# Performance work log

Hardware: AMD Instinct MI355X
Metric: run time of the kernel (lower is better)

## Reference

```python
import jax, jax.numpy as jnp
import numpy as np

B, C, H, W = 16, 512, 32, 32
NUM_HEADS = 8
GROUPS = 32
EPS = 1e-5


def setup_inputs() -> dict:
    key = jax.random.key(0)
    ks = jax.random.split(key, 3)
    x = jax.random.normal(ks[0], (B, C, H, W), dtype=jnp.float32)
    # Conv2d 1x1 weights stored as (out, in); init ~ fan-in scaled normal
    qkv_w = jax.random.normal(ks[1], (3 * C, C), dtype=jnp.float32) * (C ** -0.5)
    proj_w = jax.random.normal(ks[2], (C, C), dtype=jnp.float32) * (C ** -0.5)
    return {
        "x": x,
        "norm_w": jnp.ones((C,), jnp.float32),
        "norm_b": jnp.zeros((C,), jnp.float32),
        "qkv_w": qkv_w,
        "qkv_b": jnp.zeros((3 * C,), jnp.float32),
        "proj_w": proj_w,
        "proj_b": jnp.zeros((C,), jnp.float32),
    }


def reference(x, norm_w, norm_b, qkv_w, qkv_b, proj_w, proj_b):
    b, c, hh, ww = x.shape
    nh = NUM_HEADS
    hd = c // nh
    n = hh * ww

    # GroupNorm(32, C)
    xg = x.reshape(b, GROUPS, c // GROUPS, hh, ww)
    mean = xg.mean(axis=(2, 3, 4), keepdims=True)
    var = ((xg - mean) ** 2).mean(axis=(2, 3, 4), keepdims=True)
    hn = ((xg - mean) * jax.lax.rsqrt(var + EPS)).reshape(b, c, hh, ww)
    hn = hn * norm_w[None, :, None, None] + norm_b[None, :, None, None]

    # 1x1 conv QKV projection
    qkv = jnp.einsum('bchw,oc->bohw', hn, qkv_w) + qkv_b[None, :, None, None]
    # (B,3C,H,W) -> (B,3,nh,hd,N) -> (3,B,nh,N,hd)
    qkv = qkv.reshape(b, 3, nh, hd, n).transpose(1, 0, 2, 4, 3)
    q, k, v = qkv[0], qkv[1], qkv[2]

    scale = hd ** -0.5
    attn = jax.nn.softmax(jnp.einsum('bhnd,bhmd->bhnm', q, k) * scale, axis=-1)
    o = jnp.einsum('bhnm,bhmd->bhnd', attn, v)  # (B,nh,N,hd)
    o = o.transpose(0, 1, 3, 2).reshape(b, c, hh, ww)

    out = jnp.einsum('bchw,oc->bohw', o, proj_w) + proj_b[None, :, None, None]
    return out + x
```

## Files before the change

kernel.cpp:

```cpp
#include <hip/hip_runtime.h>
#include <cstdint>
#include <math.h>


typedef __bf16 bf16;
typedef __attribute__((ext_vector_type(8))) __bf16 bf16x8;
typedef __attribute__((ext_vector_type(4))) float f32x4;
typedef __attribute__((ext_vector_type(4))) short s16x4;

union U8 { uint4 u4; bf16x8 v; bf16 h[8]; };
union U4 { ushort4 u; bf16 h[4]; };
union UB4 { ushort4 u; s16x4 s; bf16 h[4]; };
union F4 { float4 v; float f[4]; };

typedef __attribute__((address_space(1))) void* gp1;
typedef __attribute__((address_space(3))) void* lp3;

__device__ __forceinline__ void async16(const void* g, void* l) {
  __builtin_amdgcn_global_load_lds((gp1)g, (lp3)l, 16, 0, 0);
}

#define LOG2E 1.44269504f

__global__ __launch_bounds__(256) void cvt_w(const float* __restrict__ qw,
                                             const float* __restrict__ pw,
                                             bf16* __restrict__ qwb,
                                             bf16* __restrict__ pwb) {
  int i = blockIdx.x * 256 + threadIdx.x;
  F4 v; bf16* dst;
  if (i < 196608) { v.v = ((const float4*)qw)[i]; dst = qwb + (size_t)i * 4; }
  else { v.v = ((const float4*)pw)[i - 196608]; dst = pwb + (size_t)(i - 196608) * 4; }
  U4 o;
#pragma unroll
  for (int j = 0; j < 4; j++) o.h[j] = (bf16)v.f[j];
  *(ushort4*)dst = o.u;
}

__global__ __launch_bounds__(256) void gn_stats(const float* __restrict__ x,
                                                float2* __restrict__ stats) {
  int bg = blockIdx.x;
  const float* base = x + (size_t)bg * 16384;
  int t = threadIdx.x;
  float s = 0.f, ss = 0.f;
#pragma unroll
  for (int p = 0; p < 16; p++) {
    F4 u; u.v = *(const float4*)(base + (size_t)(p * 256 + t) * 4);
#pragma unroll
    for (int i = 0; i < 4; i++) { float v = u.f[i]; s += v; ss += v * v; }
  }
  for (int off = 1; off < 64; off <<= 1) { s += __shfl_xor(s, off); ss += __shfl_xor(ss, off); }
  __shared__ float red[8];
  int w = t >> 6;
  if ((t & 63) == 0) { red[w] = s; red[4 + w] = ss; }
  __syncthreads();
  if (t == 0) {
    float S = red[0] + red[1] + red[2] + red[3];
    float SS = red[4] + red[5] + red[6] + red[7];
    float mean = S * (1.f / 16384.f);
    float var = SS * (1.f / 16384.f) - mean * mean;
    stats[bg] = make_float2(mean, rsqrtf(var + 1e-5f));
  }
}

__global__ __launch_bounds__(256) void gn_apply(const float* __restrict__ x,
                                                const float* __restrict__ nwp,
                                                const float* __restrict__ nbp,
                                                const float2* __restrict__ stats,
                                                bf16* __restrict__ hnt) {
  int b = blockIdx.z, nt = blockIdx.y, ct = blockIdx.x;
  int t = threadIdx.x, w = t >> 6, l = t & 63;
  int wc = w & 1, wn = w >> 1;
  int cb = ct * 128 + wc * 64 + (l & 7) * 8;
  int n0 = nt * 64 + wn * 32 + (l >> 3) * 4;
  float2 ms = stats[b * 32 + (cb >> 4)];
  float wgt[8], bia[8];
#pragma unroll
  for (int i = 0; i < 8; i++) {
    float wi = nwp[cb + i] * ms.y;
    wgt[i] = wi;
    bia[i] = nbp[cb + i] - ms.x * wi;
  }
  F4 in[8];
  const float* xb = x + ((size_t)b * 512 + cb) * 1024 + n0;
#pragma unroll
  for (int i = 0; i < 8; i++) in[i].v = *(const float4*)(xb + (size_t)i * 1024);
  bf16* ob = hnt + ((size_t)b * 1024 + n0) * 512 + cb;
#pragma unroll
  for (int j = 0; j < 4; j++) {
    U8 o;
#pragma unroll
    for (int i = 0; i < 8; i++) o.h[i] = (bf16)(in[i].f[j] * wgt[i] + bia[i]);
    *(uint4*)(ob + (size_t)j * 512) = o.u4;
  }
}

__device__ __forceinline__ void gemm_bt_core(const bf16* ga0, const bf16* gb0,
                                             bf16* At, bf16* Bt,
                                             f32x4 (&acc)[4][4], int w, int l) {
  const bf16* ga = ga0 + (size_t)(w * 16 + (l >> 2)) * 512 + (l & 3) * 8;
  const bf16* gb = gb0 + (size_t)(w * 16 + (l >> 2)) * 512 + (l & 3) * 8;
  int wr = w >> 1, wc = w & 1;
  const bf16* Ab = At + (wr * 64 + (l & 15)) * 32 + (l >> 4) * 8;
  const bf16* Bb = Bt + (wc * 64 + (l & 15)) * 32 + (l >> 4) * 8;
  bf16* lA = At + w * 16 * 32;
  bf16* lB = Bt + w * 16 * 32;
  for (int k0 = 0; k0 < 512; k0 += 32) {
    async16(ga + k0, lA);
    async16(ga + 64 * 512 + k0, lA + 64 * 32);
    async16(gb + k0, lB);
    async16(gb + 64 * 512 + k0, lB + 64 * 32);
    __syncthreads();
    bf16x8 af[4], bfr[4];
#pragma unroll
    for (int i = 0; i < 4; i++) {
      af[i] = *(const bf16x8*)(Ab + i * 512);
      bfr[i] = *(const bf16x8*)(Bb + i * 512);
    }
#pragma unroll
    for (int i = 0; i < 4; i++)
#pragma unroll
      for (int j = 0; j < 4; j++)
        acc[i][j] = __builtin_amdgcn_mfma_f32_16x16x32_bf16(af[i], bfr[j], acc[i][j], 0, 0, 0);
    __syncthreads();
  }
}

__global__ __launch_bounds__(256, 2) void qkv_gemm(const bf16* __restrict__ hnt,
                                                   const bf16* __restrict__ qwb,
                                                   const float* __restrict__ qb,
                                                   bf16* __restrict__ qsw,
                                                   bf16* __restrict__ ksw,
                                                   bf16* __restrict__ vsw) {
  __shared__ bf16 At[128 * 32];
  __shared__ bf16 Bt[128 * 32];
  int b = blockIdx.z, mt = blockIdx.y, ot = blockIdx.x;
  int m0 = mt * 128, o0 = ot * 128;
  int t = threadIdx.x, w = t >> 6, l = t & 63;
  f32x4 acc[4][4] = {};
  gemm_bt_core(hnt + ((size_t)b * 1024 + m0) * 512, qwb + (size_t)o0 * 512, At, Bt, acc, w, l);

  int wr = w >> 1, wc = w & 1, quad = l >> 4, li = l & 15;
#pragma unroll
  for (int i = 0; i < 4; i++) {
    int gnb = m0 + wr * 64 + i * 16;
    int blk = gnb >> 4;
#pragma unroll
    for (int j = 0; j < 4; j++) {
      int go = o0 + wc * 64 + j * 16 + li;
      float bias = qb[go];
      if (ot < 8) {
        int c = (ot < 4) ? go : (go - 512);
        int hh = c >> 6, d = c & 63;
        int ks = d >> 5, dq = (d >> 3) & 3, jj = d & 7;
        bf16* base = ((ot < 4) ? qsw : ksw) + ((size_t)(b * 8 + hh) << 16)
                     + (blk * 2 + ks) * 512 + dq * 8 + jj;
#pragma unroll
        for (int r = 0; r < 4; r++)
          base[(quad * 4 + r) * 32] = (bf16)(acc[i][j][r] + bias);
      } else {
        int c = go - 1024;
        int hh = c >> 6, d = c & 63;
        int df = d >> 4, lv = d & 15;
        bf16* base = vsw + ((size_t)(b * 8 + hh) << 16)
                     + (blk * 4 + df) * 256 + (lv * 4 + quad) * 4;
        U4 pk;
#pragma unroll
        for (int r = 0; r < 4; r++) pk.h[r] = (bf16)(acc[i][j][r] + bias);
        *(ushort4*)base = pk.u;
      }
    }
  }
}

__device__ __forceinline__ void attn_body(const bf16* __restrict__ kp,
                                          const bf16* __restrict__ vp, int c,
                                          U8 (&ka)[2], U8 (&kc)[2],
                                          U8 (&nka)[2], U8 (&nkc)[2],
                                          const bf16x8 (&qfr)[2][2],
                                          float (&mrun)[2], f32x4 (&lacc)[2],
                                          f32x4 (&of)[4][2]) {
  int cb = c * 2048;
  UB4 va[2][4];
#pragma unroll
  for (int kf = 0; kf < 2; kf++)
#pragma unroll
    for (int df = 0; df < 4; df++)
      va[kf][df].u = *(const ushort4*)(vp + cb + kf * 1024 + df * 256);
  f32x4 st[2][2] = {};
  __builtin_amdgcn_s_setprio(1);
#pragma unroll
  for (int kf = 0; kf < 2; kf++) {
    st[0][kf] = __builtin_amdgcn_mfma_f32_16x16x32_bf16(ka[kf].v, qfr[0][0], st[0][kf], 0, 0, 0);
    st[1][kf] = __builtin_amdgcn_mfma_f32_16x16x32_bf16(ka[kf].v, qfr[1][0], st[1][kf], 0, 0, 0);
    st[0][kf] = __builtin_amdgcn_mfma_f32_16x16x32_bf16(kc[kf].v, qfr[0][1], st[0][kf], 0, 0, 0);
    st[1][kf] = __builtin_amdgcn_mfma_f32_16x16x32_bf16(kc[kf].v, qfr[1][1], st[1][kf], 0, 0, 0);
  }
  __builtin_amdgcn_s_setprio(0);
  int cn = ((c + 1) & 31) * 2048;
#pragma unroll
  for (int kf = 0; kf < 2; kf++) {
    nka[kf].u4 = *(const uint4*)(kp + cn + kf * 1024);
    nkc[kf].u4 = *(const uint4*)(kp + cn + kf * 1024 + 512);
  }
  UB4 pfr[2][2];
#pragma unroll
  for (int qf = 0; qf < 2; qf++) {
    float mt = fmaxf(fmaxf(fmaxf(st[qf][0][0], st[qf][0][1]),
                           fmaxf(st[qf][0][2], st[qf][0][3])),
                     fmaxf(fmaxf(st[qf][1][0], st[qf][1][1]),
                           fmaxf(st[qf][1][2], st[qf][1][3])));
    if (__ballot(mt > mrun[qf] + 8.f)) {
      mt = fmaxf(mt, __shfl_xor(mt, 16));
      mt = fmaxf(mt, __shfl_xor(mt, 32));
      float mnew = fmaxf(mrun[qf], mt);
      float alpha = __builtin_amdgcn_exp2f(mrun[qf] - mnew);
      mrun[qf] = mnew;
#pragma unroll
      for (int r = 0; r < 4; r++) lacc[qf][r] *= alpha;
#pragma unroll
      for (int df = 0; df < 4; df++)
#pragma unroll
        for (int r = 0; r < 4; r++) of[df][qf][r] *= alpha;
    }
    float m = mrun[qf];
#pragma unroll
    for (int kf = 0; kf < 2; kf++)
#pragma unroll
      for (int r = 0; r < 4; r++) {
        float e = __builtin_amdgcn_exp2f(st[qf][kf][r] - m);
        lacc[qf][r] += e;
        pfr[qf][kf].h[r] = (bf16)e;
      }
  }
  __builtin_amdgcn_s_setprio(1);
#pragma unroll
  for (int kf = 0; kf < 2; kf++)
#pragma unroll
    for (int df = 0; df < 4; df++)
#pragma unroll
      for (int qf = 0; qf < 2; qf++)
        of[df][qf] = __builtin_amdgcn_mfma_f32_16x16x16bf16_1k(va[kf][df].s, pfr[qf][kf].s, of[df][qf], 0, 0, 0);
  __builtin_amdgcn_s_setprio(0);
}

__global__ __launch_bounds__(256, 4) void attn(const bf16* __restrict__ qsw,
                                               const bf16* __restrict__ ksw,
                                               const bf16* __restrict__ vsw,
                                               bf16* __restrict__ ont) {
  int bh = blockIdx.x;
  int b = bh >> 3, h = bh & 7;
  int qt = blockIdx.y;
  int t = threadIdx.x, w = t >> 6, l = t & 63;
  int quad = l >> 4, li = l & 15;
  int q0 = qt * 128 + w * 32;

  int laneK = (li * 4 + quad) * 8;
  int laneV = (li * 4 + quad) * 4;
  const bf16* qp = qsw + ((size_t)bh << 16) + laneK;
  const bf16* kp = ksw + ((size_t)bh << 16) + laneK;
  const bf16* vp = vsw + ((size_t)bh << 16) + laneV;

  const float QS = 0.125f * LOG2E;
  bf16x8 qfr[2][2];
#pragma unroll
  for (int qf = 0; qf < 2; qf++)
#pragma unroll
    for (int ks = 0; ks < 2; ks++) {
      U8 u;
      u.u4 = *(const uint4*)(qp + (((q0 >> 4) + qf) * 2 + ks) * 512);
#pragma unroll
      for (int i = 0; i < 8; i++) u.h[i] = (bf16)((float)u.h[i] * QS);
      qfr[qf][ks] = u.v;
    }

  float mrun[2] = {-INFINITY, -INFINITY};
  f32x4 lacc[2] = {};
  f32x4 of[4][2] = {};

  U8 ka0[2], kc0[2], ka1[2], kc1[2];
#pragma unroll
  for (int kf = 0; kf < 2; kf++) {
    ka0[kf].u4 = *(const uint4*)(kp + kf * 1024);
    kc0[kf].u4 = *(const uint4*)(kp + kf * 1024 + 512);
  }

  for (int c = 0; c < 32; c += 2) {
    attn_body(kp, vp, c,     ka0, kc0, ka1, kc1, qfr, mrun, lacc, of);
    attn_body(kp, vp, c + 1, ka1, kc1, ka0, kc0, qfr, mrun, lacc, of);
  }

#pragma unroll
  for (int qf = 0; qf < 2; qf++) {
    float lsum = (lacc[qf][0] + lacc[qf][1]) + (lacc[qf][2] + lacc[qf][3]);
    lsum += __shfl_xor(lsum, 16);
    lsum += __shfl_xor(lsum, 32);
    float inv = 1.f / lsum;
    bf16* ob = ont + ((size_t)b * 1024 + q0 + qf * 16 + li) * 512 + h * 64 + quad * 4;
#pragma unroll
    for (int df = 0; df < 4; df++) {
      U4 pk;
#pragma unroll
      for (int r = 0; r < 4; r++) pk.h[r] = (bf16)(of[df][qf][r] * inv);
      *(ushort4*)(ob + df * 16) = pk.u;
    }
  }
}

__global__ __launch_bounds__(256, 2) void proj_gemm(const bf16* __restrict__ ont,
                                                    const bf16* __restrict__ pwb,
                                                    const float* __restrict__ pb,
                                                    const float* __restrict__ x,
                                                    float* __restrict__ out) {
  __shared__ bf16 At[128 * 32];
  __shared__ bf16 Bt[128 * 32];
  int b = blockIdx.z, mt = blockIdx.y, ot = blockIdx.x;
  int m0 = mt * 128, o0 = ot * 128;
  int t = threadIdx.x, w = t >> 6, l = t & 63;
  f32x4 acc[4][4] = {};
  gemm_bt_core(ont + ((size_t)b * 1024 + m0) * 512, pwb + (size_t)o0 * 512, At, Bt, acc, w, l);

  int wr = w >> 1, wc = w & 1, quad = l >> 4, li = l & 15;
#pragma unroll
  for (int i = 0; i < 4; i++) {
    int gn = m0 + wr * 64 + i * 16 + quad * 4;
#pragma unroll
    for (int j = 0; j < 4; j++) {
      int go = o0 + wc * 64 + j * 16 + li;
      float bias = pb[go];
      F4 xres; xres.v = *(const float4*)(x + ((size_t)b * 512 + go) * 1024 + gn);
      F4 o;
#pragma unroll
      for (int r = 0; r < 4; r++) o.f[r] = acc[i][j][r] + bias + xres.f[r];
      *(float4*)(out + ((size_t)b * 512 + go) * 1024 + gn) = o.v;
    }
  }
}

extern "C" void kernel_launch(void* const* d_in, const int* in_sizes, int n_in,
                              void* d_out, int out_size, void* d_ws, size_t ws_size,
                              hipStream_t stream) {
  const float* x  = (const float*)d_in[0];
  const float* nw = (const float*)d_in[1];
  const float* nb = (const float*)d_in[2];
  const float* qw = (const float*)d_in[3];
  const float* qb = (const float*)d_in[4];
  const float* pw = (const float*)d_in[5];
  const float* pb = (const float*)d_in[6];
  float* out = (float*)d_out;

  char* ws = (char*)d_ws;
  float2* stats = (float2*)ws;
  bf16* qwb = (bf16*)(ws + (64u << 10));
  bf16* pwb = (bf16*)(ws + (2u << 20));
  bf16* hnt = (bf16*)(ws + (4u << 20));
  bf16* qsw = (bf16*)(ws + (20u << 20));
  bf16* ksw = (bf16*)(ws + (36u << 20));
  bf16* vsw = (bf16*)(ws + (52u << 20));
  bf16* ont = hnt;

  cvt_w<<<1024, 256, 0, stream>>>(qw, pw, qwb, pwb);
  gn_stats<<<512, 256, 0, stream>>>(x, stats);
  gn_apply<<<dim3(4, 16, 16), 256, 0, stream>>>(x, nw, nb, stats, hnt);
  qkv_gemm<<<dim3(12, 8, 16), 256, 0, stream>>>(hnt, qwb, qb, qsw, ksw, vsw);
  attn<<<dim3(128, 8, 1), 256, 0, stream>>>(qsw, ksw, vsw, ont);
  proj_gemm<<<dim3(4, 8, 16), 256, 0, stream>>>(ont, pwb, pb, x, out);
}
```

Measured before the change: 238.3 us.

## Software-pipeline attention so QK^T of next chunk overlaps softmax of current

Restructures the flash-attention inner loop so each step computes the QK^T scores for chunk c+1 while doing softmax and PV for chunk c, with K loads prefetched two chunks ahead. A prologue computes the first chunk's scores, and a sched_barrier separates the MFMA block from the exp/max block. The aim is to hide MFMA latency behind VALU softmax work. In exchange it holds more score and K registers, which could reduce occupancy or cause spills under launch_bounds(256,4).

```diff
diff --git a/kernel.cpp b/kernel.cpp
--- a/kernel.cpp
+++ b/kernel.cpp
@@ -172,10 +172,12 @@
   }
 }
 
-__device__ __forceinline__ void attn_body(const bf16* __restrict__ kp,
+__device__ __forceinline__ void attn_step(const bf16* __restrict__ kp,
                                           const bf16* __restrict__ vp, int c,
-                                          U8 (&ka)[2], U8 (&kc)[2],
-                                          U8 (&nka)[2], U8 (&nkc)[2],
+                                          f32x4 (&stc)[2][2],
+                                          U8 (&kna)[2], U8 (&knc)[2],
+                                          f32x4 (&stn)[2][2],
+                                          U8 (&kpa)[2], U8 (&kpc)[2],
                                           const bf16x8 (&qfr)[2][2],
                                           float (&mrun)[2], f32x4 (&lacc)[2],
                                           f32x4 (&of)[4][2]) {
@@ -186,29 +188,33 @@
 #pragma unroll
     for (int df = 0; df < 4; df++)
       va[kf][df].u = *(const ushort4*)(vp + cb + kf * 1024 + df * 256);
-  f32x4 st[2][2] = {};
+  int cn = ((c + 2) & 31) * 2048;
+#pragma unroll
+  for (int kf = 0; kf < 2; kf++) {
+    kpa[kf].u4 = *(const uint4*)(kp + cn + kf * 1024);
+    kpc[kf].u4 = *(const uint4*)(kp + cn + kf * 1024 + 512);
+  }
+#pragma unroll
+  for (int qf = 0; qf < 2; qf++)
+#pragma unroll
+    for (int kf = 0; kf < 2; kf++) stn[qf][kf] = (f32x4){0.f, 0.f, 0.f, 0.f};
   __builtin_amdgcn_s_setprio(1);
 #pragma unroll
   for (int kf = 0; kf < 2; kf++) {
-    st[0][kf] = __builtin_amdgcn_mfma_f32_16x16x32_bf16(ka[kf].v, qfr[0][0], st[0][kf], 0, 0, 0);
-    st[1][kf] = __builtin_amdgcn_mfma_f32_16x16x32_bf16(ka[kf].v, qfr[1][0], st[1][kf], 0, 0, 0);
-    st[0][kf] = __builtin_amdgcn_mfma_f32_16x16x32_bf16(kc[kf].v, qfr[0][1], st[0][kf], 0, 0, 0);
-    st[1][kf] = __builtin_amdgcn_mfma_f32_16x16x32_bf16(kc[kf].v, qfr[1][1], st[1][kf], 0, 0, 0);
+    stn[0][kf] = __builtin_amdgcn_mfma_f32_16x16x32_bf16(kna[kf].v, qfr[0][0], stn[0][kf], 0, 0, 0);
+    stn[1][kf] = __builtin_amdgcn_mfma_f32_16x16x32_bf16(kna[kf].v, qfr[1][0], stn[1][kf], 0, 0, 0);
+    stn[0][kf] = __builtin_amdgcn_mfma_f32_16x16x32_bf16(knc[kf].v, qfr[0][1], stn[0][kf], 0, 0, 0);
+    stn[1][kf] = __builtin_amdgcn_mfma_f32_16x16x32_bf16(knc[kf].v, qfr[1][1], stn[1][kf], 0, 0, 0);
   }
   __builtin_amdgcn_s_setprio(0);
-  int cn = ((c + 1) & 31) * 2048;
-#pragma unroll
-  for (int kf = 0; kf < 2; kf++) {
-    nka[kf].u4 = *(const uint4*)(kp + cn + kf * 1024);
-    nkc[kf].u4 = *(const uint4*)(kp + cn + kf * 1024 + 512);
-  }
+  __builtin_amdgcn_sched_barrier(0);
   UB4 pfr[2][2];
 #pragma unroll
   for (int qf = 0; qf < 2; qf++) {
-    float mt = fmaxf(fmaxf(fmaxf(st[qf][0][0], st[qf][0][1]),
-                           fmaxf(st[qf][0][2], st[qf][0][3])),
-                     fmaxf(fmaxf(st[qf][1][0], st[qf][1][1]),
-                           fmaxf(st[qf][1][2], st[qf][1][3])));
+    float mt = fmaxf(fmaxf(fmaxf(stc[qf][0][0], stc[qf][0][1]),
+                           fmaxf(stc[qf][0][2], stc[qf][0][3])),
+                     fmaxf(fmaxf(stc[qf][1][0], stc[qf][1][1]),
+                           fmaxf(stc[qf][1][2], stc[qf][1][3])));
     if (__ballot(mt > mrun[qf] + 8.f)) {
       mt = fmaxf(mt, __shfl_xor(mt, 16));
       mt = fmaxf(mt, __shfl_xor(mt, 32));
@@ -227,7 +233,7 @@
     for (int kf = 0; kf < 2; kf++)
 #pragma unroll
       for (int r = 0; r < 4; r++) {
-        float e = __builtin_amdgcn_exp2f(st[qf][kf][r] - m);
+        float e = __builtin_amdgcn_exp2f(stc[qf][kf][r] - m);
         lacc[qf][r] += e;
         pfr[qf][kf].h[r] = (bf16)e;
       }
@@ -282,11 +288,23 @@
   for (int kf = 0; kf < 2; kf++) {
     ka0[kf].u4 = *(const uint4*)(kp + kf * 1024);
     kc0[kf].u4 = *(const uint4*)(kp + kf * 1024 + 512);
-  }
+    ka1[kf].u4 = *(const uint4*)(kp + 2048 + kf * 1024);
+    kc1[kf].u4 = *(const uint4*)(kp + 2048 + kf * 1024 + 512);
+  }
+  f32x4 st0[2][2] = {}, st1[2][2];
+  __builtin_amdgcn_s_setprio(1);
+#pragma unroll
+  for (int kf = 0; kf < 2; kf++) {
+    st0[0][kf] = __builtin_amdgcn_mfma_f32_16x16x32_bf16(ka0[kf].v, qfr[0][0], st0[0][kf], 0, 0, 0);
+    st0[1][kf] = __builtin_amdgcn_mfma_f32_16x16x32_bf16(ka0[kf].v, qfr[1][0], st0[1][kf], 0, 0, 0);
+    st0[0][kf] = __builtin_amdgcn_mfma_f32_16x16x32_bf16(kc0[kf].v, qfr[0][1], st0[0][kf], 0, 0, 0);
+    st0[1][kf] = __builtin_amdgcn_mfma_f32_16x16x32_bf16(kc0[kf].v, qfr[1][1], st0[1][kf], 0, 0, 0);
+  }
+  __builtin_amdgcn_s_setprio(0);
 
   for (int c = 0; c < 32; c += 2) {
-    attn_body(kp, vp, c,     ka0, kc0, ka1, kc1, qfr, mrun, lacc, of);
-    attn_body(kp, vp, c + 1, ka1, kc1, ka0, kc0, qfr, mrun, lacc, of);
+    attn_step(kp, vp, c,     st0, ka1, kc1, st1, ka0, kc0, qfr, mrun, lacc, of);
+    attn_step(kp, vp, c + 1, st1, ka0, kc0, st0, ka1, kc1, qfr, mrun, lacc, of);
   }
 
 #pragma unroll
```

After: 296.6 us. +24.4%, slower.

## Shrink attention tile to 16 queries per wave, doubling blocks and occupancy

Applied to the files above, without the earlier changes.

The attention kernel now gives each wave one 16-row query fragment instead of two, and launches twice as many blocks. The launch-bounds occupancy hint goes from 4 to 8. The double-buffered K register prefetch is dropped in favour of a simple loop that loads K at the start of each chunk. This cuts register pressure so more waves can run at once, but each K/V load is now reused across half as many queries, which doubles K/V traffic and removes the explicit prefetch overlap.

```diff
diff --git a/kernel.cpp b/kernel.cpp
--- a/kernel.cpp
+++ b/kernel.cpp
@@ -172,78 +172,7 @@
   }
 }
 
-__device__ __forceinline__ void attn_body(const bf16* __restrict__ kp,
-                                          const bf16* __restrict__ vp, int c,
-                                          U8 (&ka)[2], U8 (&kc)[2],
-                                          U8 (&nka)[2], U8 (&nkc)[2],
-                                          const bf16x8 (&qfr)[2][2],
-                                          float (&mrun)[2], f32x4 (&lacc)[2],
-                                          f32x4 (&of)[4][2]) {
-  int cb = c * 2048;
-  UB4 va[2][4];
-#pragma unroll
-  for (int kf = 0; kf < 2; kf++)
-#pragma unroll
-    for (int df = 0; df < 4; df++)
-      va[kf][df].u = *(const ushort4*)(vp + cb + kf * 1024 + df * 256);
-  f32x4 st[2][2] = {};
-  __builtin_amdgcn_s_setprio(1);
-#pragma unroll
-  for (int kf = 0; kf < 2; kf++) {
-    st[0][kf] = __builtin_amdgcn_mfma_f32_16x16x32_bf16(ka[kf].v, qfr[0][0], st[0][kf], 0, 0, 0);
-    st[1][kf] = __builtin_amdgcn_mfma_f32_16x16x32_bf16(ka[kf].v, qfr[1][0], st[1][kf], 0, 0, 0);
-    st[0][kf] = __builtin_amdgcn_mfma_f32_16x16x32_bf16(kc[kf].v, qfr[0][1], st[0][kf], 0, 0, 0);
-    st[1][kf] = __builtin_amdgcn_mfma_f32_16x16x32_bf16(kc[kf].v, qfr[1][1], st[1][kf], 0, 0, 0);
-  }
-  __builtin_amdgcn_s_setprio(0);
-  int cn = ((c + 1) & 31) * 2048;
-#pragma unroll
-  for (int kf = 0; kf < 2; kf++) {
-    nka[kf].u4 = *(const uint4*)(kp + cn + kf * 1024);
-    nkc[kf].u4 = *(const uint4*)(kp + cn + kf * 1024 + 512);
-  }
-  UB4 pfr[2][2];
-#pragma unroll
-  for (int qf = 0; qf < 2; qf++) {
-    float mt = fmaxf(fmaxf(fmaxf(st[qf][0][0], st[qf][0][1]),
-                           fmaxf(st[qf][0][2], st[qf][0][3])),
-                     fmaxf(fmaxf(st[qf][1][0], st[qf][1][1]),
-                           fmaxf(st[qf][1][2], st[qf][1][3])));
-    if (__ballot(mt > mrun[qf] + 8.f)) {
-      mt = fmaxf(mt, __shfl_xor(mt, 16));
-      mt = fmaxf(mt, __shfl_xor(mt, 32));
-      float mnew = fmaxf(mrun[qf], mt);
-      float alpha = __builtin_amdgcn_exp2f(mrun[qf] - mnew);
-      mrun[qf] = mnew;
-#pragma unroll
-      for (int r = 0; r < 4; r++) lacc[qf][r] *= alpha;
-#pragma unroll
-      for (int df = 0; df < 4; df++)
-#pragma unroll
-        for (int r = 0; r < 4; r++) of[df][qf][r] *= alpha;
-    }
-    float m = mrun[qf];
-#pragma unroll
-    for (int kf = 0; kf < 2; kf++)
-#pragma unroll
-      for (int r = 0; r < 4; r++) {
-        float e = __builtin_amdgcn_exp2f(st[qf][kf][r] - m);
-        lacc[qf][r] += e;
-        pfr[qf][kf].h[r] = (bf16)e;
-      }
-  }
-  __builtin_amdgcn_s_setprio(1);
-#pragma unroll
-  for (int kf = 0; kf < 2; kf++)
-#pragma unroll
-    for (int df = 0; df < 4; df++)
-#pragma unroll
-      for (int qf = 0; qf < 2; qf++)
-        of[df][qf] = __builtin_amdgcn_mfma_f32_16x16x16bf16_1k(va[kf][df].s, pfr[qf][kf].s, of[df][qf], 0, 0, 0);
-  __builtin_amdgcn_s_setprio(0);
-}
-
-__global__ __launch_bounds__(256, 4) void attn(const bf16* __restrict__ qsw,
+__global__ __launch_bounds__(256, 8) void attn(const bf16* __restrict__ qsw,
                                                const bf16* __restrict__ ksw,
                                                const bf16* __restrict__ vsw,
                                                bf16* __restrict__ ont) {
@@ -252,7 +181,7 @@
   int qt = blockIdx.y;
   int t = threadIdx.x, w = t >> 6, l = t & 63;
   int quad = l >> 4, li = l & 15;
-  int q0 = qt * 128 + w * 32;
+  int q0 = qt * 64 + w * 16;
 
   int laneK = (li * 4 + quad) * 8;
   int laneV = (li * 4 + quad) * 4;
@@ -261,48 +190,86 @@
   const bf16* vp = vsw + ((size_t)bh << 16) + laneV;
 
   const float QS = 0.125f * LOG2E;
-  bf16x8 qfr[2][2];
-#pragma unroll
-  for (int qf = 0; qf < 2; qf++)
-#pragma unroll
-    for (int ks = 0; ks < 2; ks++) {
-      U8 u;
-      u.u4 = *(const uint4*)(qp + (((q0 >> 4) + qf) * 2 + ks) * 512);
-#pragma unroll
-      for (int i = 0; i < 8; i++) u.h[i] = (bf16)((float)u.h[i] * QS);
-      qfr[qf][ks] = u.v;
-    }
-
-  float mrun[2] = {-INFINITY, -INFINITY};
-  f32x4 lacc[2] = {};
-  f32x4 of[4][2] = {};
-
-  U8 ka0[2], kc0[2], ka1[2], kc1[2];
-#pragma unroll
-  for (int kf = 0; kf < 2; kf++) {
-    ka0[kf].u4 = *(const uint4*)(kp + kf * 1024);
-    kc0[kf].u4 = *(const uint4*)(kp + kf * 1024 + 512);
-  }
-
-  for (int c = 0; c < 32; c += 2) {
-    attn_body(kp, vp, c,     ka0, kc0, ka1, kc1, qfr, mrun, lacc, of);
-    attn_body(kp, vp, c + 1, ka1, kc1, ka0, kc0, qfr, mrun, lacc, of);
-  }
-
-#pragma unroll
-  for (int qf = 0; qf < 2; qf++) {
-    float lsum = (lacc[qf][0] + lacc[qf][1]) + (lacc[qf][2] + lacc[qf][3]);
-    lsum += __shfl_xor(lsum, 16);
-    lsum += __shfl_xor(lsum, 32);
-    float inv = 1.f / lsum;
-    bf16* ob = ont + ((size_t)b * 1024 + q0 + qf * 16 + li) * 512 + h * 64 + quad * 4;
-#pragma unroll
-    for (int df = 0; df < 4; df++) {
-      U4 pk;
-#pragma unroll
-      for (int r = 0; r < 4; r++) pk.h[r] = (bf16)(of[df][qf][r] * inv);
-      *(ushort4*)(ob + df * 16) = pk.u;
-    }
+  bf16x8 qfr[2];
+#pragma unroll
+  for (int ks = 0; ks < 2; ks++) {
+    U8 u;
+    u.u4 = *(const uint4*)(qp + ((q0 >> 4) * 2 + ks) * 512);
+#pragma unroll
+    for (int i = 0; i < 8; i++) u.h[i] = (bf16)((float)u.h[i] * QS);
+    qfr[ks] = u.v;
+  }
+
+  float mrun = -INFINITY;
+  f32x4 lacc = {};
+  f32x4 of[4] = {};
+
+  for (int c = 0; c < 32; c++) {
+    int cb = c * 2048;
+    U8 ka[2], kc[2];
+#pragma unroll
+    for (int kf = 0; kf < 2; kf++) {
+      ka[kf].u4 = *(const uint4*)(kp + cb + kf * 1024);
+      kc[kf].u4 = *(const uint4*)(kp + cb + kf * 1024 + 512);
+    }
+    f32x4 st[2] = {};
+    __builtin_amdgcn_s_setprio(1);
+#pragma unroll
+    for (int kf = 0; kf < 2; kf++) {
+      st[kf] = __builtin_amdgcn_mfma_f32_16x16x32_bf16(ka[kf].v, qfr[0], st[kf], 0, 0, 0);
+      st[kf] = __builtin_amdgcn_mfma_f32_16x16x32_bf16(kc[kf].v, qfr[1], st[kf], 0, 0, 0);
+    }
+    __builtin_amdgcn_s_setprio(0);
+    UB4 va[2][4];
+#pragma unroll
+    for (int kf = 0; kf < 2; kf++)
+#pragma unroll
+      for (int df = 0; df < 4; df++)
+        va[kf][df].u = *(const ushort4*)(vp + cb + kf * 1024 + df * 256);
+    float mt = fmaxf(fmaxf(fmaxf(st[0][0], st[0][1]), fmaxf(st[0][2], st[0][3])),
+                     fmaxf(fmaxf(st[1][0], st[1][1]), fmaxf(st[1][2], st[1][3])));
+    if (__ballot(mt > mrun + 8.f)) {
+      mt = fmaxf(mt, __shfl_xor(mt, 16));
+      mt = fmaxf(mt, __shfl_xor(mt, 32));
+      float mnew = fmaxf(mrun, mt);
+      float alpha = __builtin_amdgcn_exp2f(mrun - mnew);
+      mrun = mnew;
+#pragma unroll
+      for (int r = 0; r < 4; r++) lacc[r] *= alpha;
+#pragma unroll
+      for (int df = 0; df < 4; df++)
+#pragma unroll
+        for (int r = 0; r < 4; r++) of[df][r] *= alpha;
+    }
+    UB4 pfr[2];
+#pragma unroll
+    for (int kf = 0; kf < 2; kf++)
+#pragma unroll
+      for (int r = 0; r < 4; r++) {
+        float e = __builtin_amdgcn_exp2f(st[kf][r] - mrun);
+        lacc[r] += e;
+        pfr[kf].h[r] = (bf16)e;
+      }
+    __builtin_amdgcn_s_setprio(1);
+#pragma unroll
+    for (int kf = 0; kf < 2; kf++)
+#pragma unroll
+      for (int df = 0; df < 4; df++)
+        of[df] = __builtin_amdgcn_mfma_f32_16x16x16bf16_1k(va[kf][df].s, pfr[kf].s, of[df], 0, 0, 0);
+    __builtin_amdgcn_s_setprio(0);
+  }
+
+  float lsum = (lacc[0] + lacc[1]) + (lacc[2] + lacc[3]);
+  lsum += __shfl_xor(lsum, 16);
+  lsum += __shfl_xor(lsum, 32);
+  float inv = 1.f / lsum;
+  bf16* ob = ont + ((size_t)b * 1024 + q0 + li) * 512 + h * 64 + quad * 4;
+#pragma unroll
+  for (int df = 0; df < 4; df++) {
+    U4 pk;
+#pragma unroll
+    for (int r = 0; r < 4; r++) pk.h[r] = (bf16)(of[df][r] * inv);
+    *(ushort4*)(ob + df * 16) = pk.u;
   }
 }
 
@@ -362,6 +329,6 @@
   gn_stats<<<512, 256, 0, stream>>>(x, stats);
   gn_apply<<<dim3(4, 16, 16), 256, 0, stream>>>(x, nw, nb, stats, hnt);
   qkv_gemm<<<dim3(12, 8, 16), 256, 0, stream>>>(hnt, qwb, qb, qsw, ksw, vsw);
-  attn<<<dim3(128, 8, 1), 256, 0, stream>>>(qsw, ksw, vsw, ont);
+  attn<<<dim3(128, 16, 1), 256, 0, stream>>>(qsw, ksw, vsw, ont);
   proj_gemm<<<dim3(4, 8, 16), 256, 0, stream>>>(ont, pwb, pb, x, out);
 }
```

Result: slower. 282.2 us (+18.4%).
